# Kernel optimization log

Measured on AMD Instinct MI355X. Metric: run time of the kernel, lower is better.

The kernel has to match this reference:

```python
import jax, jax.numpy as jnp
import numpy as np

N = 50000      # nodes
E = 400000     # edges (before self-loops)
D_IN = 128     # input node features
H1, C1 = 8, 64   # layer-1 heads / per-head channels (concat -> 512)
H2, C2 = 1, 16   # layer-2 heads / per-head channels (mean -> 16)
NEG_SLOPE = 0.2  # PyG GATConv default leaky-relu slope


def setup_inputs() -> dict:
    key = jax.random.key(0)
    ks = jax.random.split(key, 10)
    x = jax.random.normal(ks[0], (N, D_IN), jnp.float32)
    edge_index = jax.random.randint(ks[1], (2, E), 0, N, dtype=jnp.int32)
    s1 = D_IN ** -0.5
    s2 = (H1 * C1) ** -0.5
    return {
        "x": x,
        "edge_index": edge_index,
        "W1": jax.random.normal(ks[2], (D_IN, H1 * C1), jnp.float32) * s1,
        "a1_src": jax.random.normal(ks[3], (H1, C1), jnp.float32) * (C1 ** -0.5),
        "a1_dst": jax.random.normal(ks[4], (H1, C1), jnp.float32) * (C1 ** -0.5),
        "b1": jnp.zeros((H1 * C1,), jnp.float32),
        "W2": jax.random.normal(ks[5], (H1 * C1, H2 * C2), jnp.float32) * s2,
        "a2_src": jax.random.normal(ks[6], (H2, C2), jnp.float32) * (C2 ** -0.5),
        "a2_dst": jax.random.normal(ks[7], (H2, C2), jnp.float32) * (C2 ** -0.5),
        "b2": jnp.zeros((C2,), jnp.float32),
    }


def gat_layer(x, W, a_src, a_dst, bias, src, dst, H, C, concat):
    n = x.shape[0]
    h = (x @ W).reshape(n, H, C)                       # [N,H,C]
    # per-node attention halves (PyG: alpha = a_src . h_src + a_dst . h_dst)
    al_src = jnp.einsum('nhc,hc->nh', h, a_src)        # [N,H]
    al_dst = jnp.einsum('nhc,hc->nh', h, a_dst)
    logits = jax.nn.leaky_relu(al_src[src] + al_dst[dst], NEG_SLOPE)  # [E,H]
    # segment softmax over incoming edges of each destination node
    m = jax.ops.segment_max(logits, dst, num_segments=n)
    e = jnp.exp(logits - m[dst])
    denom = jax.ops.segment_sum(e, dst, num_segments=n)
    alpha = e / denom[dst]                             # [E,H]
    out = jax.ops.segment_sum(alpha[:, :, None] * h[src], dst, num_segments=n)  # [N,H,C]
    out = out.reshape(n, H * C) if concat else out.mean(axis=1)
    return out + bias


def reference(x, edge_index, W1, a1_src, a1_dst, b1, W2, a2_src, a2_dst, b2):
    n = x.shape[0]
    # PyG GATConv adds self-loops by default (applied in each layer)
    loops = jnp.arange(n, dtype=edge_index.dtype)
    src = jnp.concatenate([edge_index[0], loops])
    dst = jnp.concatenate([edge_index[1], loops])
    h1 = gat_layer(x, W1, a1_src, a1_dst, b1, src, dst, H1, C1, True)   # [N,512]
    h1 = jax.nn.elu(h1)
    return gat_layer(h1, W2, a2_src, a2_dst, b2, src, dst, H2, C2, False)  # [N,16]
```

## Files before the change

kernel.cpp:

```cpp
#include <hip/hip_runtime.h>
#include <math.h>

#define N_NODES 50000
#define N_EDGES 400000
#define N_TOT   450000
#define NEG 0.2f
#define CAP 64

typedef __attribute__((ext_vector_type(8))) short bf16x8;
typedef __attribute__((ext_vector_type(4))) float f32x4;

__device__ __forceinline__ float lrelu(float x) { return x > 0.f ? x : NEG * x; }

__device__ __forceinline__ unsigned short f2bf(float f) {
    unsigned u = __float_as_uint(f);
    unsigned r = u + 0x7FFFu + ((u >> 16) & 1u);
    return (unsigned short)(r >> 16);
}
__device__ __forceinline__ float bf2f(unsigned short h) {
    return __uint_as_float(((unsigned)h) << 16);
}

__global__ void k_init(const float* __restrict__ W1, unsigned short* W1hiT,
                       const float* __restrict__ W2, unsigned short* W2hiT,
                       const float* __restrict__ a1s, const float* __restrict__ a1d,
                       unsigned short* W1aThi, unsigned short* W1aTlo,
                       int* cursor) {
    int i = blockIdx.x * 256 + threadIdx.x;
    if (i < 128 * 512) {
        int col = i & 511, k = i >> 9;
        W1hiT[col * 128 + k] = f2bf(W1[k * 512 + col]);
    } else if (i < 128 * 512 + 512 * 16) {
        int j = i - 128 * 512;
        int col = j & 15, k = j >> 4;
        W2hiT[col * 512 + k] = f2bf(W2[k * 16 + col]);
    } else if (i < 128 * 512 + 512 * 16 + 128 * 16) {
        int j = i - (128 * 512 + 512 * 16);
        int c16 = j & 15, k = j >> 4;
        int hd = c16 & 7;
        const float* av = (c16 < 8) ? a1s : a1d;
        float acc = 0.f;
#pragma unroll 8
        for (int c = 0; c < 64; c++)
            acc = fmaf(W1[k * 512 + hd * 64 + c], av[hd * 64 + c], acc);
        unsigned short h = f2bf(acc);
        W1aThi[c16 * 128 + k] = h;
        W1aTlo[c16 * 128 + k] = f2bf(acc - bf2f(h));
    } else {
        int j = i - (128 * 512 + 512 * 16 + 128 * 16);
        if (j < N_NODES) cursor[j] = 0;
    }
}

#define SCAT 256
__global__ __launch_bounds__(256) void k_sg1(const int* __restrict__ ei,
                                             int* __restrict__ cursor,
                                             int* __restrict__ colsrc,
                                             const float* __restrict__ x,
                                             const unsigned short* __restrict__ W1hiT,
                                             const unsigned short* __restrict__ W1aThi,
                                             const unsigned short* __restrict__ W1aTlo,
                                             unsigned short* __restrict__ h1b,
                                             float* __restrict__ al1s,
                                             float* __restrict__ al1d) {
    __shared__ unsigned short xs_hi[64 * 136];
    if (blockIdx.x < SCAT) {
        int gtid = blockIdx.x * 256 + threadIdx.x;
        for (int i = gtid; i < N_TOT; i += SCAT * 256) {
            int src, dst;
            if (i < N_EDGES) { src = ei[i]; dst = ei[N_EDGES + i]; }
            else             { src = dst = i - N_EDGES; }
            int pos = atomicAdd(&cursor[dst], 1);
            if (pos < CAP) colsrc[dst * CAP + pos] = src;
        }
        return;
    }
    const int t = threadIdx.x;
    const int rb = (blockIdx.x - SCAT) * 64;

#pragma unroll
    for (int i = 0; i < 8; i++) {
        int idx = t + 256 * i;
        int r = idx >> 5;
        int k = (idx & 31) * 4;
        int gr = rb + r;
        float4 v = make_float4(0.f, 0.f, 0.f, 0.f);
        if (gr < N_NODES) v = *reinterpret_cast<const float4*>(&x[gr * 128 + k]);
        ushort4 hi;
        hi.x = f2bf(v.x); hi.y = f2bf(v.y); hi.z = f2bf(v.z); hi.w = f2bf(v.w);
        *reinterpret_cast<ushort4*>(&xs_hi[r * 136 + k]) = hi;
    }
    __syncthreads();

    const int lane = t & 63;
    const int w = t >> 6;
    const int kbase = (lane >> 4) * 8;
    const int colloc = (w << 4) + (lane & 15);

#pragma unroll
    for (int pr = 0; pr < 4; pr++) {
        bf16x8 bhi[2][4];
#pragma unroll
        for (int si = 0; si < 2; si++) {
            int col = (pr * 2 + si) * 64 + colloc;
#pragma unroll
            for (int kc = 0; kc < 4; kc++)
                bhi[si][kc] = *reinterpret_cast<const bf16x8*>(&W1hiT[col * 128 + kc * 32 + kbase]);
        }
#pragma unroll
        for (int mt = 0; mt < 4; mt++) {
            const int arow = mt * 16 + (lane & 15);
            bf16x8 ah[4];
#pragma unroll
            for (int kc = 0; kc < 4; kc++)
                ah[kc] = *reinterpret_cast<const bf16x8*>(&xs_hi[arow * 136 + kc * 32 + kbase]);
#pragma unroll
            for (int si = 0; si < 2; si++) {
                f32x4 acc = {0.f, 0.f, 0.f, 0.f};
#pragma unroll
                for (int kc = 0; kc < 4; kc++)
                    acc = __builtin_amdgcn_mfma_f32_16x16x32_bf16(ah[kc], bhi[si][kc], acc, 0, 0, 0);
                const int col = (pr * 2 + si) * 64 + colloc;
                const int r0 = rb + mt * 16 + (lane >> 4) * 4;
#pragma unroll
                for (int r = 0; r < 4; r++) {
                    int row = r0 + r;
                    if (row < N_NODES) h1b[row * 512 + col] = f2bf(acc[r]);
                }
            }
        }
    }

    {
        const int c16 = lane & 15;
        bf16x8 bh[4], bl[4];
#pragma unroll
        for (int kc = 0; kc < 4; kc++) {
            bh[kc] = *reinterpret_cast<const bf16x8*>(&W1aThi[c16 * 128 + kc * 32 + kbase]);
            bl[kc] = *reinterpret_cast<const bf16x8*>(&W1aTlo[c16 * 128 + kc * 32 + kbase]);
        }
        const int arow = (w << 4) + (lane & 15);
        f32x4 acc = {0.f, 0.f, 0.f, 0.f};
#pragma unroll
        for (int kc = 0; kc < 4; kc++) {
            bf16x8 ah = *reinterpret_cast<const bf16x8*>(&xs_hi[arow * 136 + kc * 32 + kbase]);
            acc = __builtin_amdgcn_mfma_f32_16x16x32_bf16(ah, bh[kc], acc, 0, 0, 0);
            acc = __builtin_amdgcn_mfma_f32_16x16x32_bf16(ah, bl[kc], acc, 0, 0, 0);
        }
        const int r0 = rb + (w << 4) + (lane >> 4) * 4;
#pragma unroll
        for (int r = 0; r < 4; r++) {
            int row = r0 + r;
            if (row < N_NODES) {
                if (c16 < 8) al1s[row * 8 + c16] = acc[r];
                else         al1d[row * 8 + (c16 - 8)] = acc[r];
            }
        }
    }
}

__global__ __launch_bounds__(256) void k_agg1(const int* __restrict__ cursor,
                                              const int* __restrict__ colsrc,
                                              const float* __restrict__ al1s,
                                              const float* __restrict__ al1d,
                                              const unsigned short* __restrict__ h1b,
                                              const float* __restrict__ b1,
                                              unsigned short* __restrict__ h1a) {
    __shared__ float pw[4][8 * 65];
    int wid = threadIdx.x >> 6;
    int lane = threadIdx.x & 63;
    int n = blockIdx.x * 4 + wid;
    if (n >= N_NODES) return;
    int cnt = min(cursor[n], CAP);
    const int eb = n * CAP;
    const float4 d0 = *reinterpret_cast<const float4*>(&al1d[n * 8]);
    const float4 d1 = *reinterpret_cast<const float4*>(&al1d[n * 8 + 4]);
    int hA = lane >> 4, hB = hA + 4;
    int cA = 4 * lane, cB = 256 + 4 * lane;
    f32x4 aA = {0.f, 0.f, 0.f, 0.f}, aB = {0.f, 0.f, 0.f, 0.f};
    float sA = 0.f, sB = 0.f;
    float* mypw = pw[wid];

    int s0 = 0;
    float p[8];
    if (lane < cnt) {
        s0 = colsrc[eb + lane];
        const float4 u0 = *reinterpret_cast<const float4*>(&al1s[s0 * 8]);
        const float4 u1 = *reinterpret_cast<const float4*>(&al1s[s0 * 8 + 4]);
        p[0] = __expf(fminf(lrelu(u0.x + d0.x), 60.f));
        p[1] = __expf(fminf(lrelu(u0.y + d0.y), 60.f));
        p[2] = __expf(fminf(lrelu(u0.z + d0.z), 60.f));
        p[3] = __expf(fminf(lrelu(u0.w + d0.w), 60.f));
        p[4] = __expf(fminf(lrelu(u1.x + d1.x), 60.f));
        p[5] = __expf(fminf(lrelu(u1.y + d1.y), 60.f));
        p[6] = __expf(fminf(lrelu(u1.z + d1.z), 60.f));
        p[7] = __expf(fminf(lrelu(u1.w + d1.w), 60.f));
    } else {
#pragma unroll
        for (int h = 0; h < 8; h++) p[h] = 0.f;
    }
#pragma unroll
    for (int h = 0; h < 8; h++) mypw[h * 65 + lane] = p[h];

    for (int j = 0; j < cnt; j++) {
        int s = __shfl(s0, j, 64);
        float wA = mypw[hA * 65 + j];
        float wB = mypw[hB * 65 + j];
        ushort4 hvA = *reinterpret_cast<const ushort4*>(&h1b[s * 512 + cA]);
        ushort4 hvB = *reinterpret_cast<const ushort4*>(&h1b[s * 512 + cB]);
        sA += wA; sB += wB;
        aA[0] = fmaf(wA, bf2f(hvA.x), aA[0]);
        aA[1] = fmaf(wA, bf2f(hvA.y), aA[1]);
        aA[2] = fmaf(wA, bf2f(hvA.z), aA[2]);
        aA[3] = fmaf(wA, bf2f(hvA.w), aA[3]);
        aB[0] = fmaf(wB, bf2f(hvB.x), aB[0]);
        aB[1] = fmaf(wB, bf2f(hvB.y), aB[1]);
        aB[2] = fmaf(wB, bf2f(hvB.z), aB[2]);
        aB[3] = fmaf(wB, bf2f(hvB.w), aB[3]);
    }
    float iA = 1.f / sA, iB = 1.f / sB;
    const float4 bA = *reinterpret_cast<const float4*>(&b1[cA]);
    const float4 bB = *reinterpret_cast<const float4*>(&b1[cB]);
    float vA[4], vB[4];
    vA[0] = aA[0] * iA + bA.x; vA[1] = aA[1] * iA + bA.y;
    vA[2] = aA[2] * iA + bA.z; vA[3] = aA[3] * iA + bA.w;
    vB[0] = aB[0] * iB + bB.x; vB[1] = aB[1] * iB + bB.y;
    vB[2] = aB[2] * iB + bB.z; vB[3] = aB[3] * iB + bB.w;
#pragma unroll
    for (int k = 0; k < 4; k++) {
        vA[k] = vA[k] > 0.f ? vA[k] : __expf(vA[k]) - 1.f;
        vB[k] = vB[k] > 0.f ? vB[k] : __expf(vB[k]) - 1.f;
    }
    ushort4 oA, oB;
    oA.x = f2bf(vA[0]); oA.y = f2bf(vA[1]); oA.z = f2bf(vA[2]); oA.w = f2bf(vA[3]);
    oB.x = f2bf(vB[0]); oB.y = f2bf(vB[1]); oB.z = f2bf(vB[2]); oB.w = f2bf(vB[3]);
    *reinterpret_cast<ushort4*>(&h1a[n * 512 + cA]) = oA;
    *reinterpret_cast<ushort4*>(&h1a[n * 512 + cB]) = oB;
}

__global__ __launch_bounds__(256) void k_gemm2(const unsigned short* __restrict__ h1a,
                                               const unsigned short* __restrict__ W2hiT,
                                               const float* __restrict__ a2s,
                                               const float* __restrict__ a2d,
                                               unsigned short* __restrict__ h2b,
                                               float* __restrict__ al2s,
                                               float* __restrict__ al2d) {
    __shared__ unsigned short as_hi[64 * 520];
    const int t = threadIdx.x;
    const int rb = blockIdx.x * 64;

#pragma unroll
    for (int i = 0; i < 16; i++) {
        int idx = t + 256 * i;
        int r = idx >> 6;
        int k8 = (idx & 63) * 8;
        int gr = rb + r;
        uint4 v = make_uint4(0, 0, 0, 0);
        if (gr < N_NODES) v = *reinterpret_cast<const uint4*>(&h1a[gr * 512 + k8]);
        *reinterpret_cast<uint4*>(&as_hi[r * 520 + k8]) = v;
    }
    __syncthreads();

    const int lane = t & 63;
    const int w = t >> 6;
    const int col = lane & 15;
    const int kbase = (lane >> 4) * 8;
    const int arow = (w << 4) + (lane & 15);

    f32x4 acc = {0.f, 0.f, 0.f, 0.f};
#pragma unroll
    for (int kc = 0; kc < 16; kc++) {
        bf16x8 bh = *reinterpret_cast<const bf16x8*>(&W2hiT[col * 512 + kc * 32 + kbase]);
        bf16x8 ah = *reinterpret_cast<const bf16x8*>(&as_hi[arow * 520 + kc * 32 + kbase]);
        acc = __builtin_amdgcn_mfma_f32_16x16x32_bf16(ah, bh, acc, 0, 0, 0);
    }
    const float as_c = a2s[col];
    const float ad_c = a2d[col];
    const int rloc = (w << 4) + (lane >> 4) * 4;
#pragma unroll
    for (int r = 0; r < 4; r++) {
        int row = rb + rloc + r;
        float ps = acc[r] * as_c;
        float pd = acc[r] * ad_c;
        ps += __shfl_xor(ps, 1, 64); pd += __shfl_xor(pd, 1, 64);
        ps += __shfl_xor(ps, 2, 64); pd += __shfl_xor(pd, 2, 64);
        ps += __shfl_xor(ps, 4, 64); pd += __shfl_xor(pd, 4, 64);
        ps += __shfl_xor(ps, 8, 64); pd += __shfl_xor(pd, 8, 64);
        if (row < N_NODES) {
            h2b[row * 16 + col] = f2bf(acc[r]);
            if ((lane & 15) == 0) { al2s[row] = ps; al2d[row] = pd; }
        }
    }
}

__global__ __launch_bounds__(256) void k_agg2(const int* __restrict__ cursor,
                                              const int* __restrict__ colsrc,
                                              const float* __restrict__ al2s,
                                              const float* __restrict__ al2d,
                                              const unsigned short* __restrict__ h2b,
                                              const float* __restrict__ b2,
                                              float* __restrict__ out) {
    int wv = threadIdx.x >> 6, lane = threadIdx.x & 63;
    int n = blockIdx.x * 4 + wv;
    if (n >= N_NODES) return;
    int cnt = min(cursor[n], CAP);
    const int eb = n * CAP;
    float ald = al2d[n];
    int c = lane & 15, q = lane >> 4;
    float acc = 0.f, smL = 0.f;
    int e = q;
    for (; e + 4 < cnt; e += 8) {
        int s0 = colsrc[eb + e];
        int s1 = colsrc[eb + e + 4];
        float w0 = __expf(fminf(lrelu(al2s[s0] + ald), 60.f));
        float w1 = __expf(fminf(lrelu(al2s[s1] + ald), 60.f));
        unsigned short v0 = h2b[s0 * 16 + c];
        unsigned short v1 = h2b[s1 * 16 + c];
        smL += w0 + w1;
        acc = fmaf(w0, bf2f(v0), acc);
        acc = fmaf(w1, bf2f(v1), acc);
    }
    for (; e < cnt; e += 4) {
        int s = colsrc[eb + e];
        float w = __expf(fminf(lrelu(al2s[s] + ald), 60.f));
        smL += w;
        acc = fmaf(w, bf2f(h2b[s * 16 + c]), acc);
    }
    acc += __shfl_xor(acc, 16, 64); smL += __shfl_xor(smL, 16, 64);
    acc += __shfl_xor(acc, 32, 64); smL += __shfl_xor(smL, 32, 64);
    if (q == 0) out[n * 16 + c] = acc / smL + b2[c];
}

extern "C" void kernel_launch(void* const* d_in, const int* in_sizes, int n_in,
                              void* d_out, int out_size, void* d_ws, size_t ws_size,
                              hipStream_t stream) {
    const float* x   = (const float*)d_in[0];
    const int*   ei  = (const int*)d_in[1];
    const float* W1  = (const float*)d_in[2];
    const float* a1s = (const float*)d_in[3];
    const float* a1d = (const float*)d_in[4];
    const float* b1  = (const float*)d_in[5];
    const float* W2  = (const float*)d_in[6];
    const float* a2s = (const float*)d_in[7];
    const float* a2d = (const float*)d_in[8];
    const float* b2  = (const float*)d_in[9];
    float* out = (float*)d_out;

    char* ws = (char*)d_ws;
    unsigned short* h1b = (unsigned short*)(ws + 0);
    unsigned short* h1a = (unsigned short*)(ws + 51200000);
    unsigned short* h2b = (unsigned short*)(ws + 102400000);
    float* al1s = (float*)(ws + 105600000);
    float* al1d = (float*)(ws + 107200000);
    float* al2s = (float*)(ws + 108800000);
    float* al2d = (float*)(ws + 109000000);
    int* cursor = (int*)(ws + 109200000);
    int* colsrc = (int*)(ws + 109400000);
    unsigned short* W1hiT  = (unsigned short*)(ws + 122200000);
    unsigned short* W2hiT  = (unsigned short*)(ws + 122336000);
    unsigned short* W1aThi = (unsigned short*)(ws + 122352384);
    unsigned short* W1aTlo = (unsigned short*)(ws + 122356480);

    k_init<<<492, 256, 0, stream>>>(W1, W1hiT, W2, W2hiT, a1s, a1d, W1aThi, W1aTlo, cursor);

    k_sg1<<<SCAT + (N_NODES + 63) / 64, 256, 0, stream>>>(ei, cursor, colsrc, x,
                                                          W1hiT, W1aThi, W1aTlo,
                                                          h1b, al1s, al1d);

    k_agg1<<<(N_NODES + 3) / 4, 256, 0, stream>>>(cursor, colsrc, al1s, al1d, h1b, b1, h1a);

    k_gemm2<<<(N_NODES + 63) / 64, 256, 0, stream>>>(h1a, W2hiT, a2s, a2d, h2b, al2s, al2d);
    k_agg2<<<(N_NODES + 3) / 4, 256, 0, stream>>>(cursor, colsrc, al2s, al2d, h2b, b2, out);
}
```

Baseline: 247.3 us.

## Fuse layer-2 projection GEMM into layer-1 aggregation kernel

The layer-2 GEMM (512->16 projection plus attention logits) moves into the layer-1 aggregation kernel. Each block's four aggregated rows are staged in shared memory and one wave runs the MFMA over them, which removes the h1a round trip through global memory and one kernel launch. The aggregation loop is also reorganised so each lane owns 8 contiguous channels of one head, loads 16 bytes per neighbour and unrolls four neighbours at a time. In exchange, the MFMA tile is mostly padding (4 valid rows of 16), three waves sit idle at a block-wide barrier, and the early return for n >= N_NODES is dropped, which is only safe because N is divisible by 4.

```diff
diff --git a/kernel.cpp b/kernel.cpp
--- a/kernel.cpp
+++ b/kernel.cpp
@@ -8,6 +8,7 @@
 #define CAP 64
 
 typedef __attribute__((ext_vector_type(8))) short bf16x8;
+typedef __attribute__((ext_vector_type(8))) unsigned short u16x8;
 typedef __attribute__((ext_vector_type(4))) float f32x4;
 
 __device__ __forceinline__ float lrelu(float x) { return x > 0.f ? x : NEG * x; }
@@ -165,21 +166,26 @@
                                               const float* __restrict__ al1d,
                                               const unsigned short* __restrict__ h1b,
                                               const float* __restrict__ b1,
-                                              unsigned short* __restrict__ h1a) {
-    __shared__ float pw[4][8 * 65];
-    int wid = threadIdx.x >> 6;
-    int lane = threadIdx.x & 63;
-    int n = blockIdx.x * 4 + wid;
-    if (n >= N_NODES) return;
-    int cnt = min(cursor[n], CAP);
+                                              const unsigned short* __restrict__ W2hiT,
+                                              const float* __restrict__ a2s,
+                                              const float* __restrict__ a2d,
+                                              unsigned short* __restrict__ h2b,
+                                              float* __restrict__ al2s,
+                                              float* __restrict__ al2d) {
+    __shared__ float pw[4][8 * 66];
+    __shared__ __align__(16) unsigned short vs[4 * 520];
+    const int wid  = threadIdx.x >> 6;
+    const int lane = threadIdx.x & 63;
+    const int n0 = blockIdx.x * 4;
+    const int n  = n0 + wid;
+    const int cnt = min(cursor[n], CAP);
     const int eb = n * CAP;
+    const int h  = lane >> 3;
+    const int c8 = lane << 3;
+    float* mypw = pw[wid];
+
     const float4 d0 = *reinterpret_cast<const float4*>(&al1d[n * 8]);
     const float4 d1 = *reinterpret_cast<const float4*>(&al1d[n * 8 + 4]);
-    int hA = lane >> 4, hB = hA + 4;
-    int cA = 4 * lane, cB = 256 + 4 * lane;
-    f32x4 aA = {0.f, 0.f, 0.f, 0.f}, aB = {0.f, 0.f, 0.f, 0.f};
-    float sA = 0.f, sB = 0.f;
-    float* mypw = pw[wid];
 
     int s0 = 0;
     float p[8];
@@ -197,98 +203,90 @@
         p[7] = __expf(fminf(lrelu(u1.w + d1.w), 60.f));
     } else {
 #pragma unroll
-        for (int h = 0; h < 8; h++) p[h] = 0.f;
-    }
-#pragma unroll
-    for (int h = 0; h < 8; h++) mypw[h * 65 + lane] = p[h];
-
-    for (int j = 0; j < cnt; j++) {
+        for (int hh = 0; hh < 8; hh++) p[hh] = 0.f;
+    }
+#pragma unroll
+    for (int hh = 0; hh < 8; hh++) mypw[hh * 66 + lane] = p[hh];
+
+    float acc[8] = {0.f, 0.f, 0.f, 0.f, 0.f, 0.f, 0.f, 0.f};
+    float sm = 0.f;
+    const int pwh = h * 66;
+
+    int j = 0;
+    for (; j + 3 < cnt; j += 4) {
+        int sa = __shfl(s0, j,     64);
+        int sb = __shfl(s0, j + 1, 64);
+        int sc = __shfl(s0, j + 2, 64);
+        int sd = __shfl(s0, j + 3, 64);
+        u16x8 va = *reinterpret_cast<const u16x8*>(&h1b[sa * 512 + c8]);
+        u16x8 vb = *reinterpret_cast<const u16x8*>(&h1b[sb * 512 + c8]);
+        u16x8 vc = *reinterpret_cast<const u16x8*>(&h1b[sc * 512 + c8]);
+        u16x8 vd = *reinterpret_cast<const u16x8*>(&h1b[sd * 512 + c8]);
+        float wa = mypw[pwh + j];
+        float wb = mypw[pwh + j + 1];
+        float wc = mypw[pwh + j + 2];
+        float wd = mypw[pwh + j + 3];
+        sm += (wa + wb) + (wc + wd);
+#pragma unroll
+        for (int k = 0; k < 8; k++) {
+            float t0 = fmaf(wa, bf2f(va[k]), acc[k]);
+            t0 = fmaf(wb, bf2f(vb[k]), t0);
+            t0 = fmaf(wc, bf2f(vc[k]), t0);
+            acc[k] = fmaf(wd, bf2f(vd[k]), t0);
+        }
+    }
+    for (; j < cnt; ++j) {
         int s = __shfl(s0, j, 64);
-        float wA = mypw[hA * 65 + j];
-        float wB = mypw[hB * 65 + j];
-        ushort4 hvA = *reinterpret_cast<const ushort4*>(&h1b[s * 512 + cA]);
-        ushort4 hvB = *reinterpret_cast<const ushort4*>(&h1b[s * 512 + cB]);
-        sA += wA; sB += wB;
-        aA[0] = fmaf(wA, bf2f(hvA.x), aA[0]);
-        aA[1] = fmaf(wA, bf2f(hvA.y), aA[1]);
-        aA[2] = fmaf(wA, bf2f(hvA.z), aA[2]);
-        aA[3] = fmaf(wA, bf2f(hvA.w), aA[3]);
-        aB[0] = fmaf(wB, bf2f(hvB.x), aB[0]);
-        aB[1] = fmaf(wB, bf2f(hvB.y), aB[1]);
-        aB[2] = fmaf(wB, bf2f(hvB.z), aB[2]);
-        aB[3] = fmaf(wB, bf2f(hvB.w), aB[3]);
-    }
-    float iA = 1.f / sA, iB = 1.f / sB;
-    const float4 bA = *reinterpret_cast<const float4*>(&b1[cA]);
-    const float4 bB = *reinterpret_cast<const float4*>(&b1[cB]);
-    float vA[4], vB[4];
-    vA[0] = aA[0] * iA + bA.x; vA[1] = aA[1] * iA + bA.y;
-    vA[2] = aA[2] * iA + bA.z; vA[3] = aA[3] * iA + bA.w;
-    vB[0] = aB[0] * iB + bB.x; vB[1] = aB[1] * iB + bB.y;
-    vB[2] = aB[2] * iB + bB.z; vB[3] = aB[3] * iB + bB.w;
-#pragma unroll
-    for (int k = 0; k < 4; k++) {
-        vA[k] = vA[k] > 0.f ? vA[k] : __expf(vA[k]) - 1.f;
-        vB[k] = vB[k] > 0.f ? vB[k] : __expf(vB[k]) - 1.f;
-    }
-    ushort4 oA, oB;
-    oA.x = f2bf(vA[0]); oA.y = f2bf(vA[1]); oA.z = f2bf(vA[2]); oA.w = f2bf(vA[3]);
-    oB.x = f2bf(vB[0]); oB.y = f2bf(vB[1]); oB.z = f2bf(vB[2]); oB.w = f2bf(vB[3]);
-    *reinterpret_cast<ushort4*>(&h1a[n * 512 + cA]) = oA;
-    *reinterpret_cast<ushort4*>(&h1a[n * 512 + cB]) = oB;
-}
-
-__global__ __launch_bounds__(256) void k_gemm2(const unsigned short* __restrict__ h1a,
-                                               const unsigned short* __restrict__ W2hiT,
-                                               const float* __restrict__ a2s,
-                                               const float* __restrict__ a2d,
-                                               unsigned short* __restrict__ h2b,
-                                               float* __restrict__ al2s,
-                                               float* __restrict__ al2d) {
-    __shared__ unsigned short as_hi[64 * 520];
-    const int t = threadIdx.x;
-    const int rb = blockIdx.x * 64;
-
-#pragma unroll
-    for (int i = 0; i < 16; i++) {
-        int idx = t + 256 * i;
-        int r = idx >> 6;
-        int k8 = (idx & 63) * 8;
-        int gr = rb + r;
-        uint4 v = make_uint4(0, 0, 0, 0);
-        if (gr < N_NODES) v = *reinterpret_cast<const uint4*>(&h1a[gr * 512 + k8]);
-        *reinterpret_cast<uint4*>(&as_hi[r * 520 + k8]) = v;
-    }
+        u16x8 v = *reinterpret_cast<const u16x8*>(&h1b[s * 512 + c8]);
+        float w = mypw[pwh + j];
+        sm += w;
+#pragma unroll
+        for (int k = 0; k < 8; k++) acc[k] = fmaf(w, bf2f(v[k]), acc[k]);
+    }
+
+    const float inv = 1.f / sm;
+    const float4 ba = *reinterpret_cast<const float4*>(&b1[c8]);
+    const float4 bb = *reinterpret_cast<const float4*>(&b1[c8 + 4]);
+    float v[8];
+    v[0] = acc[0] * inv + ba.x; v[1] = acc[1] * inv + ba.y;
+    v[2] = acc[2] * inv + ba.z; v[3] = acc[3] * inv + ba.w;
+    v[4] = acc[4] * inv + bb.x; v[5] = acc[5] * inv + bb.y;
+    v[6] = acc[6] * inv + bb.z; v[7] = acc[7] * inv + bb.w;
+#pragma unroll
+    for (int k = 0; k < 8; k++)
+        v[k] = v[k] > 0.f ? v[k] : __expf(v[k]) - 1.f;
+    u16x8 o;
+#pragma unroll
+    for (int k = 0; k < 8; k++) o[k] = f2bf(v[k]);
+    *reinterpret_cast<u16x8*>(&vs[wid * 520 + c8]) = o;
+
     __syncthreads();
 
-    const int lane = t & 63;
-    const int w = t >> 6;
-    const int col = lane & 15;
-    const int kbase = (lane >> 4) * 8;
-    const int arow = (w << 4) + (lane & 15);
-
-    f32x4 acc = {0.f, 0.f, 0.f, 0.f};
-#pragma unroll
-    for (int kc = 0; kc < 16; kc++) {
-        bf16x8 bh = *reinterpret_cast<const bf16x8*>(&W2hiT[col * 512 + kc * 32 + kbase]);
-        bf16x8 ah = *reinterpret_cast<const bf16x8*>(&as_hi[arow * 520 + kc * 32 + kbase]);
-        acc = __builtin_amdgcn_mfma_f32_16x16x32_bf16(ah, bh, acc, 0, 0, 0);
-    }
-    const float as_c = a2s[col];
-    const float ad_c = a2d[col];
-    const int rloc = (w << 4) + (lane >> 4) * 4;
-#pragma unroll
-    for (int r = 0; r < 4; r++) {
-        int row = rb + rloc + r;
-        float ps = acc[r] * as_c;
-        float pd = acc[r] * ad_c;
-        ps += __shfl_xor(ps, 1, 64); pd += __shfl_xor(pd, 1, 64);
-        ps += __shfl_xor(ps, 2, 64); pd += __shfl_xor(pd, 2, 64);
-        ps += __shfl_xor(ps, 4, 64); pd += __shfl_xor(pd, 4, 64);
-        ps += __shfl_xor(ps, 8, 64); pd += __shfl_xor(pd, 8, 64);
-        if (row < N_NODES) {
-            h2b[row * 16 + col] = f2bf(acc[r]);
-            if ((lane & 15) == 0) { al2s[row] = ps; al2d[row] = pd; }
+    if (wid == 0) {
+        const int col   = lane & 15;
+        const int kbase = (lane >> 4) << 3;
+        const int rowm  = lane & 3;
+        f32x4 a2 = {0.f, 0.f, 0.f, 0.f};
+#pragma unroll 4
+        for (int kc = 0; kc < 16; kc++) {
+            bf16x8 bh = *reinterpret_cast<const bf16x8*>(&W2hiT[col * 512 + kc * 32 + kbase]);
+            bf16x8 ah = *reinterpret_cast<const bf16x8*>(&vs[rowm * 520 + kc * 32 + kbase]);
+            a2 = __builtin_amdgcn_mfma_f32_16x16x32_bf16(ah, bh, a2, 0, 0, 0);
+        }
+        if (lane < 16) {
+            const float as_c = a2s[col];
+            const float ad_c = a2d[col];
+#pragma unroll
+            for (int r = 0; r < 4; r++) {
+                float ps = a2[r] * as_c;
+                float pd = a2[r] * ad_c;
+                ps += __shfl_xor(ps, 1, 64); pd += __shfl_xor(pd, 1, 64);
+                ps += __shfl_xor(ps, 2, 64); pd += __shfl_xor(pd, 2, 64);
+                ps += __shfl_xor(ps, 4, 64); pd += __shfl_xor(pd, 4, 64);
+                ps += __shfl_xor(ps, 8, 64); pd += __shfl_xor(pd, 8, 64);
+                h2b[(n0 + r) * 16 + col] = f2bf(a2[r]);
+                if (lane == 0) { al2s[n0 + r] = ps; al2d[n0 + r] = pd; }
+            }
         }
     }
 }
@@ -348,7 +346,6 @@
 
     char* ws = (char*)d_ws;
     unsigned short* h1b = (unsigned short*)(ws + 0);
-    unsigned short* h1a = (unsigned short*)(ws + 51200000);
     unsigned short* h2b = (unsigned short*)(ws + 102400000);
     float* al1s = (float*)(ws + 105600000);
     float* al1d = (float*)(ws + 107200000);
@@ -367,8 +364,8 @@
                                                           W1hiT, W1aThi, W1aTlo,
                                                           h1b, al1s, al1d);
 
-    k_agg1<<<(N_NODES + 3) / 4, 256, 0, stream>>>(cursor, colsrc, al1s, al1d, h1b, b1, h1a);
-
-    k_gemm2<<<(N_NODES + 63) / 64, 256, 0, stream>>>(h1a, W2hiT, a2s, a2d, h2b, al2s, al2d);
+    k_agg1<<<(N_NODES + 3) / 4, 256, 0, stream>>>(cursor, colsrc, al1s, al1d, h1b, b1,
+                                                  W2hiT, a2s, a2d, h2b, al2s, al2d);
+
     k_agg2<<<(N_NODES + 3) / 4, 256, 0, stream>>>(cursor, colsrc, al2s, al2d, h2b, b2, out);
 }
```

New measurement: 218.8 us. 1.13x faster.
